# Kernel tuning notes

Measured on AMD Instinct MI355X. Metric: run time of the kernel, lower is better.

Reference implementation:

```python
import jax, jax.numpy as jnp
import numpy as np

# Poincare ball, curvature c = 1.0 (manifold.c)
C = 1.0
SQC = 1.0  # sqrt(C)
EPS = 1e-15
BALL_EPS = 1e-5
ALPHA = 0.1  # params[0]


def _project(x):
    # clip points back inside the open ball
    norm = jnp.linalg.norm(x, axis=-1, keepdims=True)
    maxnorm = (1.0 - BALL_EPS) / SQC
    return jnp.where(norm > maxnorm, x / jnp.maximum(norm, EPS) * maxnorm, x)


def _artanh(x):
    return jnp.arctanh(jnp.clip(x, -1.0 + 1e-7, 1.0 - 1e-7))


def _lambda_x(x):
    # conformal factor lambda_x = 2 / (1 - c||x||^2)
    return 2.0 / jnp.maximum(1.0 - C * jnp.sum(x * x, axis=-1, keepdims=True), EPS)


def _mobius_scalar_mul(r, x):
    n = jnp.maximum(jnp.linalg.norm(x, axis=-1, keepdims=True), EPS)
    return jnp.tanh(r * _artanh(SQC * n)) * x / (SQC * n)


def _mobius_add(x, y):
    x2 = jnp.sum(x * x, axis=-1, keepdims=True)
    y2 = jnp.sum(y * y, axis=-1, keepdims=True)
    xy = jnp.sum(x * y, axis=-1, keepdims=True)
    num = (1.0 + 2.0 * C * xy + C * y2) * x + (1.0 - C * x2) * y
    den = 1.0 + 2.0 * C * xy + C * C * x2 * y2
    return num / jnp.maximum(den, EPS)


def _expmap0(u):
    n = jnp.maximum(jnp.linalg.norm(u, axis=-1, keepdims=True), EPS)
    return jnp.tanh(SQC * n) * u / (SQC * n)


def _mobius_matvec(W, x):
    # Mobius matrix-vector multiply: expmap0-style rescale of x @ W^T
    xn = jnp.maximum(jnp.linalg.norm(x, axis=-1, keepdims=True), EPS)
    mx = x @ W.T
    mxn = jnp.maximum(jnp.linalg.norm(mx, axis=-1, keepdims=True), EPS)
    res = jnp.tanh(mxn / xn * _artanh(SQC * xn)) * mx / (SQC * mxn)
    return _project(res)


def _clamp_abs(x, eps=1e-10):
    return jnp.where(x >= 0, jnp.maximum(x, eps), jnp.minimum(x, -eps))


def weighted_midpoint_spmm(x, src, dst, w, n):
    # gyro-midpoint of neighbors under sparse adjacency weights
    gamma = _lambda_x(x)                                   # [N,1]
    msg = (gamma * x)[src] * w[:, None]                    # [E,d] irregular gather
    num = jax.ops.segment_sum(msg, dst, num_segments=n)    # [N,d]
    den = jax.ops.segment_sum(jnp.abs(w) * (gamma[:, 0] - 1.0)[src], dst,
                              num_segments=n)[:, None]     # [N,1]
    return _project(_mobius_scalar_mul(0.5, num / _clamp_abs(den)))


def weighted_midpoint_pair(a, b, wa, wb):
    # weighted_midpoint(stack([a,b],dim=1), weights=[wa,wb], reducedim=[1])
    ga, gb = _lambda_x(a), _lambda_x(b)
    num = wa * ga * a + wb * gb * b
    den = abs(wa) * (ga - 1.0) + abs(wb) * (gb - 1.0)
    return _project(_mobius_scalar_mul(0.5, num / _clamp_abs(den)))


def setup_inputs() -> dict:
    key = jax.random.key(0)
    kx, kh, kw, kW, kb, ks, kd = jax.random.split(key, 7)
    N, D, E = 100000, 48, 1600000

    def to_ball(u):
        # squash gaussian samples well inside the Poincare ball
        n = jnp.linalg.norm(u, axis=-1, keepdims=True)
        return 0.5 * u / (1.0 + n)

    x = to_ball(jax.random.normal(kx, (N, D), dtype=jnp.float32))
    h_init = to_ball(jax.random.normal(kh, (N, D), dtype=jnp.float32))
    edge_w = jax.random.uniform(kw, (E,), dtype=jnp.float32, minval=0.01, maxval=1.0)
    W = jax.random.normal(kW, (D, D), dtype=jnp.float32) * (1.0 / np.sqrt(D))
    bias = jax.random.normal(kb, (D,), dtype=jnp.float32) * 0.01
    edge_src = jax.random.randint(ks, (E,), 0, N, dtype=jnp.int32)
    edge_dst = jax.random.randint(kd, (E,), 0, N, dtype=jnp.int32)
    return {"x": x, "h_init": h_init, "edge_w": edge_w, "W": W, "bias": bias,
            "edge_src": edge_src, "edge_dst": edge_dst}


def reference(x, h_init, edge_w, W, bias, edge_src, edge_dst):
    n = x.shape[0]
    # 1) sparse adjacency-weighted hyperbolic midpoint aggregation
    support = weighted_midpoint_spmm(x, edge_src, edge_dst, edge_w, n)
    # 2) residual midpoint with h_init, weights [1-alpha, alpha]
    support = weighted_midpoint_pair(support, h_init, 1.0 - ALPHA, ALPHA)
    # 3) Mobius linear (HyperbolicLinearFast, eval-mode dropout, no nonlin)
    h = _mobius_matvec(W, support)
    h = _project(_mobius_add(h, _expmap0(bias[None, :])))
    return h
```

## Files before the change

### kernel.cpp

```cpp
#include <hip/hip_runtime.h>
#include <math.h>

#define D  48
#define DQ 12
#define SPAN 128
#define SHIFT 7
#define PCH  8192
#define PTH  512
#define NPB  16
#define WSTR 52
#define YROW 16

constexpr float F_EPS   = 1e-15f;
constexpr float MAXNORM = 1.0f - 1e-5f;

__device__ __forceinline__ float clampabs(float x) {
    return (x >= 0.0f) ? fmaxf(x, 1e-10f) : fminf(x, -1e-10f);
}

__device__ __forceinline__ unsigned short f2bf(float f) {
    unsigned u = __float_as_uint(f);
    u += 0x7FFFu + ((u >> 16) & 1u);
    return (unsigned short)(u >> 16);
}

__device__ __forceinline__ float bf2f(unsigned short u) {
    return __uint_as_float(((unsigned)u) << 16);
}

__device__ __forceinline__ float gm1f(ushort4 a) {
    return __uint_as_float((unsigned)a.x | ((unsigned)a.y << 16));
}

__device__ __forceinline__ float fast_tanh(float x) {
    float e = __expf(2.0f * x);
    return 1.0f - __fdividef(2.0f, e + 1.0f);
}
__device__ __forceinline__ float fast_atanh(float x) {
    x = fminf(x, 1.0f - 1e-7f);
    return 0.5f * __logf(__fdividef(1.0f + x, 1.0f - x));
}

__global__ void k_gamma(const float* __restrict__ x, float* __restrict__ gam,
                        int* __restrict__ ghist, int n, int nb)
{
    int i = blockIdx.x * blockDim.x + threadIdx.x;
    if (i < nb) ghist[i] = 0;
    if (i >= n) return;
    const float4* xr = reinterpret_cast<const float4*>(x) + (size_t)i * DQ;
    float s = 0.0f;
#pragma unroll
    for (int q = 0; q < DQ; ++q) {
        float4 v = xr[q];
        s += v.x * v.x + v.y * v.y + v.z * v.z + v.w * v.w;
    }
    gam[i] = 2.0f / fmaxf(1.0f - s, F_EPS);
}

__global__ __launch_bounds__(PTH) void k_hist(const int* __restrict__ dst,
                                              int* __restrict__ ghist, int E, int nb)
{
    __shared__ int h[1024];
    int t = threadIdx.x;
    for (int i = t; i < 1024; i += PTH) h[i] = 0;
    __syncthreads();
    int base = blockIdx.x * PCH;
#pragma unroll 4
    for (int k = 0; k < PCH / PTH; ++k) {
        int i = base + k * PTH + t;
        if (i < E) {
            unsigned b = ((unsigned)dst[i]) >> SHIFT;
            if (b < 1024u) atomicAdd(&h[b], 1);
        }
    }
    __syncthreads();
    for (int i = t; i < nb; i += PTH) {
        int c = h[i];
        if (c) atomicAdd(&ghist[i], c);
    }
}

__global__ __launch_bounds__(1024) void k_scanb(const int* __restrict__ ghist,
                                                int* __restrict__ gstart,
                                                int* __restrict__ gcur, int nb, int E)
{
    __shared__ int sh[1024];
    int t = threadIdx.x;
    int v = (t < nb) ? ghist[t] : 0;
    sh[t] = v;
    __syncthreads();
    for (int off = 1; off < 1024; off <<= 1) {
        int a = sh[t];
        int b = (t >= off) ? sh[t - off] : 0;
        __syncthreads();
        sh[t] = a + b;
        __syncthreads();
    }
    if (t < nb) { int s = sh[t] - v; gstart[t] = s; gcur[t] = s; }
    if (t == 0) gstart[nb] = E;
}

__global__ __launch_bounds__(PTH) void k_part(const int* __restrict__ src,
                                              const int* __restrict__ dst,
                                              const float* __restrict__ w,
                                              int* __restrict__ gcur,
                                              int2* __restrict__ seg, int E, int nb)
{
    __shared__ int hist[1024];
    __shared__ int base_[1024];
    __shared__ int lcur[1024];
    int t = threadIdx.x;
    for (int i = t; i < 1024; i += PTH) { hist[i] = 0; base_[i] = 0; lcur[i] = 0; }
    __syncthreads();
    int b0 = blockIdx.x * PCH;
#pragma unroll 4
    for (int k = 0; k < PCH / PTH; ++k) {
        int i = b0 + k * PTH + t;
        if (i < E) {
            unsigned b = ((unsigned)dst[i]) >> SHIFT;
            if (b < 1024u) atomicAdd(&hist[b], 1);
        }
    }
    __syncthreads();
    for (int i = t; i < nb; i += PTH) {
        int c = hist[i];
        if (c) base_[i] = atomicAdd(&gcur[i], c);
    }
    __syncthreads();
#pragma unroll 4
    for (int k = 0; k < PCH / PTH; ++k) {
        int i = b0 + k * PTH + t;
        if (i < E) {
            int d = dst[i];
            unsigned b = ((unsigned)d) >> SHIFT;
            if (b < 1024u) {
                int pos = base_[b] + atomicAdd(&lcur[b], 1);
                if (pos >= 0 && pos < E) {
                    int2 r;
                    r.x = ((d & (SPAN - 1)) << 24) | (src[i] & 0xFFFFFF);
                    r.y = __float_as_int(w[i]);
                    seg[pos] = r;
                }
            }
        }
    }
}

__global__ __launch_bounds__(256) void k_sortb(
    const int2* __restrict__ seg, const int* __restrict__ gstart,
    int* __restrict__ starts, int2* __restrict__ seg2, int n, int E)
{
    __shared__ int hist[SPAN];
    __shared__ int sb[SPAN];
    __shared__ int cur[SPAN];
    int b = blockIdx.x;
    int t = threadIdx.x;
    if (b == 0 && t == 0) starts[n] = E;
    int segL = gstart[b], segR = gstart[b + 1];
    if (segL < 0) segL = 0;
    if (segR > E) segR = E;
    if (t < SPAN) hist[t] = 0;
    __syncthreads();
    {
        int j = segL + t;
        for (; j + 768 < segR; j += 1024) {
            unsigned d0 = ((unsigned)seg[j      ].x) >> 24;
            unsigned d1 = ((unsigned)seg[j + 256].x) >> 24;
            unsigned d2 = ((unsigned)seg[j + 512].x) >> 24;
            unsigned d3 = ((unsigned)seg[j + 768].x) >> 24;
            atomicAdd(&hist[d0], 1);
            atomicAdd(&hist[d1], 1);
            atomicAdd(&hist[d2], 1);
            atomicAdd(&hist[d3], 1);
        }
        for (; j < segR; j += 256) {
            unsigned dl = ((unsigned)seg[j].x) >> 24;
            atomicAdd(&hist[dl], 1);
        }
    }
    __syncthreads();
    if (t < SPAN) sb[t] = hist[t];
    __syncthreads();
    for (int off = 1; off < SPAN; off <<= 1) {
        int a = 0;
        if (t < SPAN) { a = sb[t]; if (t >= off) a += sb[t - off]; }
        __syncthreads();
        if (t < SPAN) sb[t] = a;
        __syncthreads();
    }
    if (t < SPAN) {
        int ls = sb[t] - hist[t];
        cur[t] = segL + ls;
        int node = b * SPAN + t;
        if (node < n) starts[node] = segL + ls;
    }
    __syncthreads();
    {
        int j = segL + t;
        for (; j + 768 < segR; j += 1024) {
            int2 r0 = seg[j      ];
            int2 r1 = seg[j + 256];
            int2 r2 = seg[j + 512];
            int2 r3 = seg[j + 768];
            int p0 = atomicAdd(&cur[((unsigned)r0.x) >> 24], 1);
            int p1 = atomicAdd(&cur[((unsigned)r1.x) >> 24], 1);
            int p2 = atomicAdd(&cur[((unsigned)r2.x) >> 24], 1);
            int p3 = atomicAdd(&cur[((unsigned)r3.x) >> 24], 1);
            if (p0 >= 0 && p0 < E) seg2[p0] = make_int2(r0.x & 0xFFFFFF, r0.y);
            if (p1 >= 0 && p1 < E) seg2[p1] = make_int2(r1.x & 0xFFFFFF, r1.y);
            if (p2 >= 0 && p2 < E) seg2[p2] = make_int2(r2.x & 0xFFFFFF, r2.y);
            if (p3 >= 0 && p3 < E) seg2[p3] = make_int2(r3.x & 0xFFFFFF, r3.y);
        }
        for (; j < segR; j += 256) {
            int2 r = seg[j];
            int pos = atomicAdd(&cur[((unsigned)r.x) >> 24], 1);
            if (pos >= 0 && pos < E) seg2[pos] = make_int2(r.x & 0xFFFFFF, r.y);
        }
    }
}

__global__ __launch_bounds__(256) void k_prep(const float* __restrict__ x,
                                              const float* __restrict__ gam,
                                              ushort4* __restrict__ ybf, int n)
{
    long long t = (long long)blockIdx.x * blockDim.x + threadIdx.x;
    int node = (int)(t / YROW);
    if (node >= n) return;
    int slot = (int)(t % YROW);
    float g = gam[node];
    ushort4 o;
    if (slot < 12) {
        float4 v = reinterpret_cast<const float4*>(x)[(size_t)node * DQ + slot];
        o.x = f2bf(v.x * g);
        o.y = f2bf(v.y * g);
        o.z = f2bf(v.z * g);
        o.w = f2bf(v.w * g);
    } else if (slot == 12) {
        unsigned u = __float_as_uint(g - 1.0f);
        o.x = (unsigned short)(u & 0xFFFFu);
        o.y = (unsigned short)(u >> 16);
        o.z = 0; o.w = 0;
    } else {
        o.x = 0; o.y = 0; o.z = 0; o.w = 0;
    }
    ybf[(size_t)node * YROW + slot] = o;
}

__global__ __launch_bounds__(256) void k_fuse(
    const ushort4* __restrict__ ybf,
    const int* __restrict__ starts,
    const int2* __restrict__ srec,
    const float* __restrict__ h_init,
    const float* __restrict__ Wm,
    const float* __restrict__ bias,
    float* __restrict__ out, int n, int E)
{
    __shared__ float Ws[D * WSTR];
    __shared__ float bs[D];
    __shared__ float aLds[NPB][WSTR];
    int t = threadIdx.x;
    for (int k = t; k < D * D; k += 256) Ws[(k / D) * WSTR + (k % D)] = Wm[k];
    if (t < D) bs[t] = bias[t];

    int grp = t >> 4;
    int lane = t & 15;
    int i = blockIdx.x * NPB + grp;
    bool act = (i < n);

    auto gsum = [](float v) {
        v += __shfl_xor(v, 1, 16);
        v += __shfl_xor(v, 2, 16);
        v += __shfl_xor(v, 4, 16);
        v += __shfl_xor(v, 8, 16);
        return v;
    };
    auto hmp_scale = [](float s) {
        float nrm = sqrtf(s);
        float ncl = fmaxf(nrm, F_EPS);
        float m = fminf(ncl, 1.0f - 1e-7f);
        float sc = __fdividef(__fdividef(m, ncl),
                              1.0f + sqrtf(fmaxf(1.0f - m * m, 0.0f)));
        float rn = nrm * sc;
        if (rn > MAXNORM) sc *= MAXNORM / fmaxf(rn, F_EPS);
        return sc;
    };

    int j0 = 0, j1 = 0;
    if (act) {
        j0 = starts[i]; j1 = starts[i + 1];
        if (j0 < 0) j0 = 0;
        if (j1 > E) j1 = E;
    }
    int pp = (lane < 12) ? lane : 12;
    float4 acc = make_float4(0.f, 0.f, 0.f, 0.f);
    float dacc = 0.f;
    int j = j0;
    for (; j + 3 < j1; j += 4) {
        int2 r0 = srec[j];
        int2 r1 = srec[j + 1];
        int2 r2 = srec[j + 2];
        int2 r3 = srec[j + 3];
        ushort4 a0 = ybf[(size_t)r0.x * YROW + pp];
        ushort4 a1 = ybf[(size_t)r1.x * YROW + pp];
        ushort4 a2 = ybf[(size_t)r2.x * YROW + pp];
        ushort4 a3 = ybf[(size_t)r3.x * YROW + pp];
        float w0 = __int_as_float(r0.y);
        float w1 = __int_as_float(r1.y);
        float w2 = __int_as_float(r2.y);
        float w3 = __int_as_float(r3.y);
        if (lane < 12) {
            acc.x = fmaf(w0, bf2f(a0.x), acc.x);
            acc.y = fmaf(w0, bf2f(a0.y), acc.y);
            acc.z = fmaf(w0, bf2f(a0.z), acc.z);
            acc.w = fmaf(w0, bf2f(a0.w), acc.w);
            acc.x = fmaf(w1, bf2f(a1.x), acc.x);
            acc.y = fmaf(w1, bf2f(a1.y), acc.y);
            acc.z = fmaf(w1, bf2f(a1.z), acc.z);
            acc.w = fmaf(w1, bf2f(a1.w), acc.w);
            acc.x = fmaf(w2, bf2f(a2.x), acc.x);
            acc.y = fmaf(w2, bf2f(a2.y), acc.y);
            acc.z = fmaf(w2, bf2f(a2.z), acc.z);
            acc.w = fmaf(w2, bf2f(a2.w), acc.w);
            acc.x = fmaf(w3, bf2f(a3.x), acc.x);
            acc.y = fmaf(w3, bf2f(a3.y), acc.y);
            acc.z = fmaf(w3, bf2f(a3.z), acc.z);
            acc.w = fmaf(w3, bf2f(a3.w), acc.w);
        } else if (lane == 12) {
            dacc += fabsf(w0) * gm1f(a0) + fabsf(w1) * gm1f(a1)
                  + fabsf(w2) * gm1f(a2) + fabsf(w3) * gm1f(a3);
        }
    }
    for (; j < j1; ++j) {
        int2 r0 = srec[j];
        ushort4 a0 = ybf[(size_t)r0.x * YROW + pp];
        float w0 = __int_as_float(r0.y);
        if (lane < 12) {
            acc.x = fmaf(w0, bf2f(a0.x), acc.x);
            acc.y = fmaf(w0, bf2f(a0.y), acc.y);
            acc.z = fmaf(w0, bf2f(a0.z), acc.z);
            acc.w = fmaf(w0, bf2f(a0.w), acc.w);
        } else if (lane == 12) {
            dacc += fabsf(w0) * gm1f(a0);
        }
    }

    float dv = __shfl(dacc, 12, 16);

    if (lane < 12)
        reinterpret_cast<float4*>(&aLds[grp][0])[lane] = acc;
    __syncthreads();

    float dinv = 1.0f / clampabs(dv);
    float a0 = aLds[grp][lane]      * dinv;
    float a1 = aLds[grp][lane + 16] * dinv;
    float a2 = aLds[grp][lane + 32] * dinv;

    float s1 = gsum(a0 * a0 + a1 * a1 + a2 * a2);
    float sc1 = hmp_scale(s1);
    a0 *= sc1; a1 *= sc1; a2 *= sc1;
    float sa = s1 * sc1 * sc1;

    float s2, sc2;
    {
        float b0 = 0.f, b1 = 0.f, b2 = 0.f;
        if (act) {
            const float* hr = h_init + (size_t)i * D;
            b0 = hr[lane];
            b1 = hr[lane + 16];
            b2 = hr[lane + 32];
        }
        float sb = gsum(b0 * b0 + b1 * b1 + b2 * b2);
        float ga = 2.0f / fmaxf(1.0f - sa, F_EPS);
        float gb = 2.0f / fmaxf(1.0f - sb, F_EPS);
        const float wa = 0.9f, wb = 0.1f;
        float dinv2 = 1.0f / clampabs(wa * (ga - 1.0f) + wb * (gb - 1.0f));
        float ca = wa * ga * dinv2, cb = wb * gb * dinv2;
        a0 = ca * a0 + cb * b0;
        a1 = ca * a1 + cb * b1;
        a2 = ca * a2 + cb * b2;
        s2 = gsum(a0 * a0 + a1 * a1 + a2 * a2);
        sc2 = hmp_scale(s2);
        a0 *= sc2; a1 *= sc2; a2 *= sc2;
    }
    float xn = fmaxf(sqrtf(s2) * sc2, F_EPS);

    aLds[grp][lane]      = a0;
    aLds[grp][lane + 16] = a1;
    aLds[grp][lane + 32] = a2;
    __syncthreads();

    const float4* av4 = reinterpret_cast<const float4*>(&aLds[grp][0]);
    const float4* w04 = reinterpret_cast<const float4*>(&Ws[lane * WSTR]);
    const float4* w14 = reinterpret_cast<const float4*>(&Ws[(lane + 16) * WSTR]);
    const float4* w24 = reinterpret_cast<const float4*>(&Ws[(lane + 32) * WSTR]);
    float acc0 = 0.f, acc1 = 0.f, acc2 = 0.f;
#pragma unroll
    for (int kq = 0; kq < DQ; ++kq) {
        float4 a4 = av4[kq];
        float4 x0 = w04[kq];
        float4 x1 = w14[kq];
        float4 x2 = w24[kq];
        acc0 = fmaf(x0.x, a4.x, acc0); acc0 = fmaf(x0.y, a4.y, acc0);
        acc0 = fmaf(x0.z, a4.z, acc0); acc0 = fmaf(x0.w, a4.w, acc0);
        acc1 = fmaf(x1.x, a4.x, acc1); acc1 = fmaf(x1.y, a4.y, acc1);
        acc1 = fmaf(x1.z, a4.z, acc1); acc1 = fmaf(x1.w, a4.w, acc1);
        acc2 = fmaf(x2.x, a4.x, acc2); acc2 = fmaf(x2.y, a4.y, acc2);
        acc2 = fmaf(x2.z, a4.z, acc2); acc2 = fmaf(x2.w, a4.w, acc2);
    }
    float bl0 = bs[lane], bl1 = bs[lane + 16], bl2 = bs[lane + 32];
    float smx = gsum(acc0 * acc0 + acc1 * acc1 + acc2 * acc2);
    float xyr = gsum(acc0 * bl0 + acc1 * bl1 + acc2 * bl2);
    float bn2 = gsum(bl0 * bl0 + bl1 * bl1 + bl2 * bl2);

    float mxnr = sqrtf(smx);
    float mxn = fmaxf(mxnr, F_EPS);
    float tt = fast_tanh(__fdividef(mxn, xn) * fast_atanh(xn));
    float sc = __fdividef(tt, mxn);
    float rn = mxnr * sc;
    if (rn > MAXNORM) sc *= MAXNORM / fmaxf(rn, F_EPS);

    float bn  = fmaxf(sqrtf(bn2), F_EPS);
    float ebs = __fdividef(fast_tanh(bn), bn);
    float y2  = ebs * ebs * bn2;

    float x2v = sc * sc * smx;
    float xy = sc * ebs * xyr;
    float c1 = 1.0f + 2.0f * xy + y2;
    float c2 = 1.0f - x2v;
    float dn3 = 1.0f / fmaxf(1.0f + 2.0f * xy + x2v * y2, F_EPS);

    float s3 = dn3 * dn3 * (c1 * c1 * sc * sc * smx
                            + 2.0f * c1 * c2 * sc * ebs * xyr
                            + c2 * c2 * ebs * ebs * bn2);
    float nrm3 = sqrtf(s3);
    float fp = (nrm3 > MAXNORM) ? (MAXNORM / fmaxf(nrm3, F_EPS)) : 1.0f;

    float CA = c1 * sc * dn3 * fp;
    float CB = c2 * ebs * dn3 * fp;

    if (act) {
        float* orow = out + (size_t)i * D;
        orow[lane]      = fmaf(CA, acc0, CB * bl0);
        orow[lane + 16] = fmaf(CA, acc1, CB * bl1);
        orow[lane + 32] = fmaf(CA, acc2, CB * bl2);
    }
}

__global__ void k_init_atomic(float* __restrict__ den, float* __restrict__ num, int n)
{
    int i = blockIdx.x * blockDim.x + threadIdx.x;
    if (i >= n) return;
    den[i] = 0.0f;
    float4* nr = reinterpret_cast<float4*>(num) + (size_t)i * DQ;
    float4 z = make_float4(0.f, 0.f, 0.f, 0.f);
#pragma unroll
    for (int q = 0; q < DQ; ++q) nr[q] = z;
}

__global__ void k_edge_atomic(const float* __restrict__ x, const float* __restrict__ gam,
                              const int* __restrict__ src, const int* __restrict__ dst,
                              const float* __restrict__ w,
                              float* __restrict__ num, float* __restrict__ den, int E)
{
    long long t = (long long)blockIdx.x * blockDim.x + threadIdx.x;
    int e = (int)(t / DQ);
    if (e >= E) return;
    int part = (int)(t % DQ);
    int s = src[e];
    int d = dst[e];
    float we = w[e];
    float g  = gam[s];
    float4 xv = reinterpret_cast<const float4*>(x)[(size_t)s * DQ + part];
    float c = we * g;
    float* np_ = num + (size_t)d * D + part * 4;
    atomicAdd(np_ + 0, c * xv.x);
    atomicAdd(np_ + 1, c * xv.y);
    atomicAdd(np_ + 2, c * xv.z);
    atomicAdd(np_ + 3, c * xv.w);
    if (part == 0) atomicAdd(den + d, fabsf(we) * (g - 1.0f));
}

__global__ __launch_bounds__(256) void k_node_fb(
    float* __restrict__ out,
    const float* __restrict__ den,
    const float* __restrict__ h_init,
    const float* __restrict__ Wm,
    const float* __restrict__ bias, int n)
{
    __shared__ float Ws[D * WSTR];
    __shared__ float bs[D];
    __shared__ float aLds[NPB][WSTR];
    int t = threadIdx.x;
    for (int k = t; k < D * D; k += 256) Ws[(k / D) * WSTR + (k % D)] = Wm[k];
    if (t < D) bs[t] = bias[t];
    __syncthreads();

    int grp = t >> 4;
    int lane = t & 15;
    int i = blockIdx.x * NPB + grp;
    bool act = (i < n);

    auto gsum = [](float v) {
        v += __shfl_xor(v, 1, 16);
        v += __shfl_xor(v, 2, 16);
        v += __shfl_xor(v, 4, 16);
        v += __shfl_xor(v, 8, 16);
        return v;
    };
    auto hmp_scale = [](float s) {
        float nrm = sqrtf(s);
        float ncl = fmaxf(nrm, F_EPS);
        float m = fminf(ncl, 1.0f - 1e-7f);
        float sc = __fdividef(__fdividef(m, ncl),
                              1.0f + sqrtf(fmaxf(1.0f - m * m, 0.0f)));
        float rn = nrm * sc;
        if (rn > MAXNORM) sc *= MAXNORM / fmaxf(rn, F_EPS);
        return sc;
    };

    float a0 = 0.f, a1 = 0.f, a2 = 0.f;
    if (act) {
        float dinv = 1.0f / clampabs(den[i]);
        const float* nr = out + (size_t)i * D;
        a0 = nr[lane] * dinv;
        a1 = nr[lane + 16] * dinv;
        a2 = nr[lane + 32] * dinv;
    }
    float s1 = gsum(a0 * a0 + a1 * a1 + a2 * a2);
    float sc1 = hmp_scale(s1);
    a0 *= sc1; a1 *= sc1; a2 *= sc1;
    float sa = s1 * sc1 * sc1;

    float s2, sc2;
    {
        float b0 = 0.f, b1 = 0.f, b2 = 0.f;
        if (act) {
            const float* hr = h_init + (size_t)i * D;
            b0 = hr[lane];
            b1 = hr[lane + 16];
            b2 = hr[lane + 32];
        }
        float sb = gsum(b0 * b0 + b1 * b1 + b2 * b2);
        float ga = 2.0f / fmaxf(1.0f - sa, F_EPS);
        float gb = 2.0f / fmaxf(1.0f - sb, F_EPS);
        const float wa = 0.9f, wb = 0.1f;
        float dinv = 1.0f / clampabs(wa * (ga - 1.0f) + wb * (gb - 1.0f));
        float ca = wa * ga * dinv, cb = wb * gb * dinv;
        a0 = ca * a0 + cb * b0;
        a1 = ca * a1 + cb * b1;
        a2 = ca * a2 + cb * b2;
        s2 = gsum(a0 * a0 + a1 * a1 + a2 * a2);
        sc2 = hmp_scale(s2);
        a0 *= sc2; a1 *= sc2; a2 *= sc2;
    }
    float xn = fmaxf(sqrtf(s2) * sc2, F_EPS);

    aLds[grp][lane]      = a0;
    aLds[grp][lane + 16] = a1;
    aLds[grp][lane + 32] = a2;
    __syncthreads();

    const float4* av4 = reinterpret_cast<const float4*>(&aLds[grp][0]);
    const float4* w04 = reinterpret_cast<const float4*>(&Ws[lane * WSTR]);
    const float4* w14 = reinterpret_cast<const float4*>(&Ws[(lane + 16) * WSTR]);
    const float4* w24 = reinterpret_cast<const float4*>(&Ws[(lane + 32) * WSTR]);
    float acc0 = 0.f, acc1 = 0.f, acc2 = 0.f;
#pragma unroll
    for (int kq = 0; kq < DQ; ++kq) {
        float4 a4 = av4[kq];
        float4 x0 = w04[kq];
        float4 x1 = w14[kq];
        float4 x2 = w24[kq];
        acc0 = fmaf(x0.x, a4.x, acc0); acc0 = fmaf(x0.y, a4.y, acc0);
        acc0 = fmaf(x0.z, a4.z, acc0); acc0 = fmaf(x0.w, a4.w, acc0);
        acc1 = fmaf(x1.x, a4.x, acc1); acc1 = fmaf(x1.y, a4.y, acc1);
        acc1 = fmaf(x1.z, a4.z, acc1); acc1 = fmaf(x1.w, a4.w, acc1);
        acc2 = fmaf(x2.x, a4.x, acc2); acc2 = fmaf(x2.y, a4.y, acc2);
        acc2 = fmaf(x2.z, a4.z, acc2); acc2 = fmaf(x2.w, a4.w, acc2);
    }
    float bl0 = bs[lane], bl1 = bs[lane + 16], bl2 = bs[lane + 32];
    float smx = gsum(acc0 * acc0 + acc1 * acc1 + acc2 * acc2);
    float xyr = gsum(acc0 * bl0 + acc1 * bl1 + acc2 * bl2);
    float bn2 = gsum(bl0 * bl0 + bl1 * bl1 + bl2 * bl2);

    float mxnr = sqrtf(smx);
    float mxn = fmaxf(mxnr, F_EPS);
    float tt = fast_tanh(__fdividef(mxn, xn) * fast_atanh(xn));
    float sc = __fdividef(tt, mxn);
    float rn = mxnr * sc;
    if (rn > MAXNORM) sc *= MAXNORM / fmaxf(rn, F_EPS);

    float bn  = fmaxf(sqrtf(bn2), F_EPS);
    float ebs = __fdividef(fast_tanh(bn), bn);
    float y2  = ebs * ebs * bn2;

    float x2v = sc * sc * smx;
    float xy = sc * ebs * xyr;
    float c1 = 1.0f + 2.0f * xy + y2;
    float c2 = 1.0f - x2v;
    float dn3 = 1.0f / fmaxf(1.0f + 2.0f * xy + x2v * y2, F_EPS);

    float s3 = dn3 * dn3 * (c1 * c1 * sc * sc * smx
                            + 2.0f * c1 * c2 * sc * ebs * xyr
                            + c2 * c2 * ebs * ebs * bn2);
    float nrm3 = sqrtf(s3);
    float fp = (nrm3 > MAXNORM) ? (MAXNORM / fmaxf(nrm3, F_EPS)) : 1.0f;

    float CA = c1 * sc * dn3 * fp;
    float CB = c2 * ebs * dn3 * fp;

    if (act) {
        float* orow = out + (size_t)i * D;
        orow[lane]      = fmaf(CA, acc0, CB * bl0);
        orow[lane + 16] = fmaf(CA, acc1, CB * bl1);
        orow[lane + 32] = fmaf(CA, acc2, CB * bl2);
    }
}

extern "C" void kernel_launch(void* const* d_in, const int* in_sizes, int n_in,
                              void* d_out, int out_size, void* d_ws, size_t ws_size,
                              hipStream_t stream)
{
    const float* x      = (const float*)d_in[0];
    const float* h_init = (const float*)d_in[1];
    const float* edge_w = (const float*)d_in[2];
    const float* W      = (const float*)d_in[3];
    const float* bias   = (const float*)d_in[4];
    const int*   esrc   = (const int*)d_in[5];
    const int*   edst   = (const int*)d_in[6];
    float* out = (float*)d_out;

    int n = in_sizes[0] / D;
    int E = in_sizes[2];
    int nb = (n + SPAN - 1) >> SHIFT;

    char* p = (char*)d_ws;
    float* gam    = (float*)p;             p += (size_t)n * 4;
    float* den    = (float*)p;             p += (size_t)n * 4;
    int*   ghist  = (int*)p;               p += (size_t)nb * 4;
    int*   gstart = (int*)p;               p += (size_t)(nb + 1) * 4;
    int*   gcur   = (int*)p;               p += (size_t)nb * 4;
    int*   starts = (int*)p;               p += (size_t)(n + 1) * 4;
    p = (char*)(((uintptr_t)p + 127) & ~(uintptr_t)127);
    int2*  seg    = (int2*)p;              p += (size_t)E * 8;
    int2*  seg2   = (int2*)p;              p += (size_t)E * 8;
    size_t need1 = (size_t)(p - (char*)d_ws);
    ushort4* ybf = (ushort4*)seg;
    bool ybf_fits = ((size_t)E * 8 >= (size_t)n * YROW * 8);

    k_gamma<<<(n + 255) / 256, 256, 0, stream>>>(x, gam, ghist, n, nb);

    bool shape_ok = (nb <= 1024) && (n < (1 << 24));
    if (shape_ok && ybf_fits && need1 <= ws_size) {
        int pb = (E + PCH - 1) / PCH;
        k_hist<<<pb, PTH, 0, stream>>>(edst, ghist, E, nb);
        k_scanb<<<1, 1024, 0, stream>>>(ghist, gstart, gcur, nb, E);
        k_part<<<pb, PTH, 0, stream>>>(esrc, edst, edge_w, gcur, seg, E, nb);
        k_sortb<<<nb, 256, 0, stream>>>(seg, gstart, starts, seg2, n, E);
        long long pt = (long long)n * YROW;
        k_prep<<<(int)((pt + 255) / 256), 256, 0, stream>>>(x, gam, ybf, n);
        k_fuse<<<(n + NPB - 1) / NPB, 256, 0, stream>>>(
            ybf, starts, seg2, h_init, W, bias, out, n, E);
    } else {
        k_init_atomic<<<(n + 255) / 256, 256, 0, stream>>>(den, out, n);
        long long tot = (long long)E * DQ;
        k_edge_atomic<<<(int)((tot + 255) / 256), 256, 0, stream>>>(x, gam, esrc, edst, edge_w, out, den, E);
        k_node_fb<<<(n + NPB - 1) / NPB, 256, 0, stream>>>(out, den, h_init, W, bias, n);
    }
}
```

Before: 138.6 us.

## Fold edge denominator term into packed bf16 edge records and shrink node rows

```diff
diff --git a/kernel.cpp b/kernel.cpp
--- a/kernel.cpp
+++ b/kernel.cpp
@@ -6,10 +6,11 @@
 #define SPAN 128
 #define SHIFT 7
 #define PCH  8192
+#define HCH  2048
 #define PTH  512
 #define NPB  16
 #define WSTR 52
-#define YROW 16
+#define YROW 12
 
 constexpr float F_EPS   = 1e-15f;
 constexpr float MAXNORM = 1.0f - 1e-5f;
@@ -26,10 +27,6 @@
 
 __device__ __forceinline__ float bf2f(unsigned short u) {
     return __uint_as_float(((unsigned)u) << 16);
-}
-
-__device__ __forceinline__ float gm1f(ushort4 a) {
-    return __uint_as_float((unsigned)a.x | ((unsigned)a.y << 16));
 }
 
 __device__ __forceinline__ float fast_tanh(float x) {
@@ -64,9 +61,9 @@
     int t = threadIdx.x;
     for (int i = t; i < 1024; i += PTH) h[i] = 0;
     __syncthreads();
-    int base = blockIdx.x * PCH;
-#pragma unroll 4
-    for (int k = 0; k < PCH / PTH; ++k) {
+    int base = blockIdx.x * HCH;
+#pragma unroll
+    for (int k = 0; k < HCH / PTH; ++k) {
         int i = base + k * PTH + t;
         if (i < E) {
             unsigned b = ((unsigned)dst[i]) >> SHIFT;
@@ -103,6 +100,7 @@
 __global__ __launch_bounds__(PTH) void k_part(const int* __restrict__ src,
                                               const int* __restrict__ dst,
                                               const float* __restrict__ w,
+                                              const float* __restrict__ gam,
                                               int* __restrict__ gcur,
                                               int2* __restrict__ seg, int E, int nb)
 {
@@ -134,11 +132,16 @@
             int d = dst[i];
             unsigned b = ((unsigned)d) >> SHIFT;
             if (b < 1024u) {
+                int s = src[i];
+                float wv = w[i];
+                float g  = gam[s];
+                unsigned short wb  = f2bf(wv);
+                unsigned short wdb = f2bf(fabsf(wv) * (g - 1.0f));
                 int pos = base_[b] + atomicAdd(&lcur[b], 1);
                 if (pos >= 0 && pos < E) {
                     int2 r;
-                    r.x = ((d & (SPAN - 1)) << 24) | (src[i] & 0xFFFFFF);
-                    r.y = __float_as_int(w[i]);
+                    r.x = ((d & (SPAN - 1)) << 24) | (s & 0xFFFFFF);
+                    r.y = ((unsigned)wb << 16) | wdb;
                     seg[pos] = r;
                 }
             }
@@ -228,21 +231,12 @@
     if (node >= n) return;
     int slot = (int)(t % YROW);
     float g = gam[node];
+    float4 v = reinterpret_cast<const float4*>(x)[(size_t)node * DQ + slot];
     ushort4 o;
-    if (slot < 12) {
-        float4 v = reinterpret_cast<const float4*>(x)[(size_t)node * DQ + slot];
-        o.x = f2bf(v.x * g);
-        o.y = f2bf(v.y * g);
-        o.z = f2bf(v.z * g);
-        o.w = f2bf(v.w * g);
-    } else if (slot == 12) {
-        unsigned u = __float_as_uint(g - 1.0f);
-        o.x = (unsigned short)(u & 0xFFFFu);
-        o.y = (unsigned short)(u >> 16);
-        o.z = 0; o.w = 0;
-    } else {
-        o.x = 0; o.y = 0; o.z = 0; o.w = 0;
-    }
+    o.x = f2bf(v.x * g);
+    o.y = f2bf(v.y * g);
+    o.z = f2bf(v.z * g);
+    o.w = f2bf(v.w * g);
     ybf[(size_t)node * YROW + slot] = o;
 }
 
@@ -291,7 +285,7 @@
         if (j0 < 0) j0 = 0;
         if (j1 > E) j1 = E;
     }
-    int pp = (lane < 12) ? lane : 12;
+    int pp = (lane < 12) ? lane : (lane - 12);
     float4 acc = make_float4(0.f, 0.f, 0.f, 0.f);
     float dacc = 0.f;
     int j = j0;
@@ -304,47 +298,42 @@
         ushort4 a1 = ybf[(size_t)r1.x * YROW + pp];
         ushort4 a2 = ybf[(size_t)r2.x * YROW + pp];
         ushort4 a3 = ybf[(size_t)r3.x * YROW + pp];
-        float w0 = __int_as_float(r0.y);
-        float w1 = __int_as_float(r1.y);
-        float w2 = __int_as_float(r2.y);
-        float w3 = __int_as_float(r3.y);
-        if (lane < 12) {
-            acc.x = fmaf(w0, bf2f(a0.x), acc.x);
-            acc.y = fmaf(w0, bf2f(a0.y), acc.y);
-            acc.z = fmaf(w0, bf2f(a0.z), acc.z);
-            acc.w = fmaf(w0, bf2f(a0.w), acc.w);
-            acc.x = fmaf(w1, bf2f(a1.x), acc.x);
-            acc.y = fmaf(w1, bf2f(a1.y), acc.y);
-            acc.z = fmaf(w1, bf2f(a1.z), acc.z);
-            acc.w = fmaf(w1, bf2f(a1.w), acc.w);
-            acc.x = fmaf(w2, bf2f(a2.x), acc.x);
-            acc.y = fmaf(w2, bf2f(a2.y), acc.y);
-            acc.z = fmaf(w2, bf2f(a2.z), acc.z);
-            acc.w = fmaf(w2, bf2f(a2.w), acc.w);
-            acc.x = fmaf(w3, bf2f(a3.x), acc.x);
-            acc.y = fmaf(w3, bf2f(a3.y), acc.y);
-            acc.z = fmaf(w3, bf2f(a3.z), acc.z);
-            acc.w = fmaf(w3, bf2f(a3.w), acc.w);
-        } else if (lane == 12) {
-            dacc += fabsf(w0) * gm1f(a0) + fabsf(w1) * gm1f(a1)
-                  + fabsf(w2) * gm1f(a2) + fabsf(w3) * gm1f(a3);
-        }
+        float w0 = bf2f((unsigned short)(((unsigned)r0.y) >> 16));
+        float w1 = bf2f((unsigned short)(((unsigned)r1.y) >> 16));
+        float w2 = bf2f((unsigned short)(((unsigned)r2.y) >> 16));
+        float w3 = bf2f((unsigned short)(((unsigned)r3.y) >> 16));
+        acc.x = fmaf(w0, bf2f(a0.x), acc.x);
+        acc.y = fmaf(w0, bf2f(a0.y), acc.y);
+        acc.z = fmaf(w0, bf2f(a0.z), acc.z);
+        acc.w = fmaf(w0, bf2f(a0.w), acc.w);
+        acc.x = fmaf(w1, bf2f(a1.x), acc.x);
+        acc.y = fmaf(w1, bf2f(a1.y), acc.y);
+        acc.z = fmaf(w1, bf2f(a1.z), acc.z);
+        acc.w = fmaf(w1, bf2f(a1.w), acc.w);
+        acc.x = fmaf(w2, bf2f(a2.x), acc.x);
+        acc.y = fmaf(w2, bf2f(a2.y), acc.y);
+        acc.z = fmaf(w2, bf2f(a2.z), acc.z);
+        acc.w = fmaf(w2, bf2f(a2.w), acc.w);
+        acc.x = fmaf(w3, bf2f(a3.x), acc.x);
+        acc.y = fmaf(w3, bf2f(a3.y), acc.y);
+        acc.z = fmaf(w3, bf2f(a3.z), acc.z);
+        acc.w = fmaf(w3, bf2f(a3.w), acc.w);
+        dacc += bf2f((unsigned short)(((unsigned)r0.y) & 0xFFFF))
+              + bf2f((unsigned short)(((unsigned)r1.y) & 0xFFFF))
+              + bf2f((unsigned short)(((unsigned)r2.y) & 0xFFFF))
+              + bf2f((unsigned short)(((unsigned)r3.y) & 0xFFFF));
     }
     for (; j < j1; ++j) {
         int2 r0 = srec[j];
         ushort4 a0 = ybf[(size_t)r0.x * YROW + pp];
-        float w0 = __int_as_float(r0.y);
-        if (lane < 12) {
-            acc.x = fmaf(w0, bf2f(a0.x), acc.x);
-            acc.y = fmaf(w0, bf2f(a0.y), acc.y);
-            acc.z = fmaf(w0, bf2f(a0.z), acc.z);
-            acc.w = fmaf(w0, bf2f(a0.w), acc.w);
-        } else if (lane == 12) {
-            dacc += fabsf(w0) * gm1f(a0);
-        }
-    }
-
-    float dv = __shfl(dacc, 12, 16);
+        float w0 = bf2f((unsigned short)(((unsigned)r0.y) >> 16));
+        acc.x = fmaf(w0, bf2f(a0.x), acc.x);
+        acc.y = fmaf(w0, bf2f(a0.y), acc.y);
+        acc.z = fmaf(w0, bf2f(a0.z), acc.z);
+        acc.w = fmaf(w0, bf2f(a0.w), acc.w);
+        dacc += bf2f((unsigned short)(((unsigned)r0.y) & 0xFFFF));
+    }
+    float dv = dacc;
 
     if (lane < 12)
         reinterpret_cast<float4*>(&aLds[grp][0])[lane] = acc;
@@ -652,10 +641,9 @@
 
     bool shape_ok = (nb <= 1024) && (n < (1 << 24));
     if (shape_ok && ybf_fits && need1 <= ws_size) {
-        int pb = (E + PCH - 1) / PCH;
-        k_hist<<<pb, PTH, 0, stream>>>(edst, ghist, E, nb);
+        k_hist<<<(E + HCH - 1) / HCH, PTH, 0, stream>>>(edst, ghist, E, nb);
         k_scanb<<<1, 1024, 0, stream>>>(ghist, gstart, gcur, nb, E);
-        k_part<<<pb, PTH, 0, stream>>>(esrc, edst, edge_w, gcur, seg, E, nb);
+        k_part<<<(E + PCH - 1) / PCH, PTH, 0, stream>>>(esrc, edst, edge_w, gam, gcur, seg, E, nb);
         k_sortb<<<nb, 256, 0, stream>>>(seg, gstart, starts, seg2, n, E);
         long long pt = (long long)n * YROW;
         k_prep<<<(int)((pt + 255) / 256), 256, 0, stream>>>(x, gam, ybf, n);
```

New measurement: 141.7 us. 2.3% more time.
